# Kernel tuning notes

Measured on AMD Instinct MI355X. Metric: run time of the kernel, lower is better.

Reference implementation:

```python
import jax, jax.numpy as jnp
import numpy as np

N_NODES = 20000
N_EDGES = 320000
N_GRAPHS = 64
OBS = 64
EDGE_DIM = 16
HEADS = 4
HID = 64
NEG_SLOPE = 0.2
EPS = 1e-16


def _gat_layer(x, src, dst, edge_attr, W, We, att_src, att_dst, att_edge, b):
    """PyG GATConv (concat=True, eval mode: no dropout).
    x: [N, Fin], edge_attr: [E, De], W: [Fin, H*C], We: [De, H*C],
    att_*: [H, C], b: [H*C]. Returns [N, H*C]."""
    N = x.shape[0]
    h = (x @ W).reshape(N, HEADS, HID)                      # [N,H,C]
    he = (edge_attr @ We).reshape(-1, HEADS, HID)           # [E,H,C]
    a_src = jnp.einsum('nhc,hc->nh', h, att_src)            # [N,H]
    a_dst = jnp.einsum('nhc,hc->nh', h, att_dst)
    a_e = jnp.einsum('ehc,hc->eh', he, att_edge)            # [E,H]
    alpha = a_src[src] + a_dst[dst] + a_e                   # [E,H]
    alpha = jax.nn.leaky_relu(alpha, NEG_SLOPE)
    # segment softmax over destination neighborhoods
    m = jax.ops.segment_max(alpha, dst, num_segments=N)     # [N,H]
    m = jnp.where(jnp.isfinite(m), m, 0.0)
    ea = jnp.exp(alpha - m[dst])
    denom = jax.ops.segment_sum(ea, dst, num_segments=N)    # [N,H]
    alpha = ea / (denom[dst] + EPS)
    msg = h[src] * alpha[:, :, None]                        # [E,H,C]
    out = jax.ops.segment_sum(msg, dst, num_segments=N)     # [N,H,C]
    return out.reshape(N, HEADS * HID) + b


def _make_params(key):
    ks = jax.random.split(key, 18)
    p = {}
    dims_in = [OBS, HEADS * HID, HEADS * HID]
    for i in range(3):
        j = i * 6
        fin = dims_in[i]
        p[f'W{i+1}'] = jax.random.normal(ks[j], (fin, HEADS * HID), jnp.float32) * (1.0 / np.sqrt(fin))
        p[f'We{i+1}'] = jax.random.normal(ks[j+1], (EDGE_DIM, HEADS * HID), jnp.float32) * (1.0 / np.sqrt(EDGE_DIM))
        p[f'att_src{i+1}'] = jax.random.normal(ks[j+2], (HEADS, HID), jnp.float32) * 0.1
        p[f'att_dst{i+1}'] = jax.random.normal(ks[j+3], (HEADS, HID), jnp.float32) * 0.1
        p[f'att_edge{i+1}'] = jax.random.normal(ks[j+4], (HEADS, HID), jnp.float32) * 0.1
        p[f'b{i+1}'] = jnp.zeros((HEADS * HID,), jnp.float32)
    return p


def setup_inputs() -> dict:
    key = jax.random.key(0)
    k1, k2, k3, k4, kp = jax.random.split(key, 5)
    inp = {
        'x': jax.random.normal(k1, (N_NODES, OBS), jnp.float32),
        'edge_index': jax.random.randint(k2, (2, N_EDGES), 0, N_NODES, jnp.int64),
        'edge_attr': jax.random.normal(k3, (N_EDGES, EDGE_DIM), jnp.float32),
        'batch': jnp.sort(jax.random.randint(k4, (N_NODES,), 0, N_GRAPHS, jnp.int64)),
    }
    inp.update(_make_params(kp))
    return inp


def reference(x, edge_index, edge_attr, batch,
              W1, We1, att_src1, att_dst1, att_edge1, b1,
              W2, We2, att_src2, att_dst2, att_edge2, b2,
              W3, We3, att_src3, att_dst3, att_edge3, b3):
    src, dst = edge_index[0], edge_index[1]
    h = jax.nn.relu(_gat_layer(x, src, dst, edge_attr, W1, We1, att_src1, att_dst1, att_edge1, b1))
    h = jax.nn.relu(_gat_layer(h, src, dst, edge_attr, W2, We2, att_src2, att_dst2, att_edge2, b2))
    h = jax.nn.relu(_gat_layer(h, src, dst, edge_attr, W3, We3, att_src3, att_dst3, att_edge3, b3))
    # global mean pool over graphs
    sums = jax.ops.segment_sum(h, batch, num_segments=N_GRAPHS)      # [G, H*C]
    counts = jax.ops.segment_sum(jnp.ones((h.shape[0], 1), h.dtype), batch, num_segments=N_GRAPHS)
    pooled = sums / jnp.maximum(counts, 1.0)
    return jnp.tanh(pooled)
```

## Files before the change

kernel.cpp:

```cpp
#include <hip/hip_runtime.h>
#include <hip/hip_bf16.h>
#include <hip/hip_fp16.h>
#include <math.h>

#define N_NODES 20000
#define N_EDGES 320000
#define N_GRAPHS 64
#define OBS 64
#define EDGE_DIM 16
#define HEADS 4
#define HID 64
#define HC 256
#define NEG_SLOPE 0.2f
#define EPSF 1e-16f
#define N_SCAN_BLOCKS ((N_NODES + 255) / 256)
#define CVT_BLOCKS (N_NODES * OBS / 4 / 256)

typedef _Float16 f16x8 __attribute__((ext_vector_type(8)));
typedef float f32x4 __attribute__((ext_vector_type(4)));

__global__ __launch_bounds__(256) void zero3_kernel(int* __restrict__ counts,
                                                    float* __restrict__ pooled,
                                                    int* __restrict__ gcounts) {
    int i = blockIdx.x * 256 + threadIdx.x;
    if (i < N_NODES) counts[i] = 0;
    if (i < N_GRAPHS * HC) pooled[i] = 0.f;
    if (i < N_GRAPHS) gcounts[i] = 0;
}

__global__ __launch_bounds__(256) void cvtwt_kernel(const float* __restrict__ x, __half* __restrict__ x16,
                                                    const float* __restrict__ W0, const float* __restrict__ W1,
                                                    const float* __restrict__ W2,
                                                    __half* __restrict__ wt0, __half* __restrict__ wt1,
                                                    __half* __restrict__ wt2) {
    int b = blockIdx.x, t = threadIdx.x;
    if (b < CVT_BLOCKS) {
        int i = (b * 256 + t) * 4;
        float4 v = *(const float4*)(x + i);
        *(__half2*)(x16 + i)     = __floats2half2_rn(v.x, v.y);
        *(__half2*)(x16 + i + 2) = __floats2half2_rn(v.z, v.w);
    } else if (b < CVT_BLOCKS + OBS) {
        int k = b - CVT_BLOCKS;
        wt0[(size_t)t * OBS + k] = __float2half(W0[(size_t)k * HC + t]);
    } else if (b < CVT_BLOCKS + OBS + HC) {
        int k = b - CVT_BLOCKS - OBS;
        wt1[(size_t)t * HC + k] = __float2half(W1[(size_t)k * HC + t]);
    } else {
        int k = b - CVT_BLOCKS - OBS - HC;
        wt2[(size_t)t * HC + k] = __float2half(W2[(size_t)k * HC + t]);
    }
}

__global__ __launch_bounds__(256) void count_kernel(const int* __restrict__ ei, int* __restrict__ counts) {
    int e = blockIdx.x * 256 + threadIdx.x;
    if (e >= N_EDGES) return;
    atomicAdd(&counts[ei[N_EDGES + e]], 1);
}

__global__ __launch_bounds__(256) void scan_local_kernel(const int* __restrict__ counts,
                                                         int* __restrict__ row_start,
                                                         int* __restrict__ blk_tot) {
    int b = blockIdx.x, t = threadIdx.x;
    int i = b * 256 + t;
    int v = (i < N_NODES) ? counts[i] : 0;
    int lane = t & 63, w = t >> 6;
    int x = v;
    #pragma unroll
    for (int off = 1; off < 64; off <<= 1) {
        int y = __shfl_up(x, off, 64);
        if (lane >= off) x += y;
    }
    __shared__ int wsum[4];
    __shared__ int woff[4];
    if (lane == 63) wsum[w] = x;
    __syncthreads();
    if (t == 0) {
        int s = 0;
        #pragma unroll
        for (int k = 0; k < 4; ++k) { woff[k] = s; s += wsum[k]; }
        blk_tot[b] = s;
    }
    __syncthreads();
    if (i < N_NODES) row_start[i] = x - v + woff[w];
}

__global__ __launch_bounds__(256) void scan_add_kernel(int* __restrict__ row_start,
                                                       const int* __restrict__ blk_tot,
                                                       int* __restrict__ cursor) {
    __shared__ int sd[128];
    int b = blockIdx.x, t = threadIdx.x;
    if (t < 128) sd[t] = (t < b && t < N_SCAN_BLOCKS) ? blk_tot[t] : 0;
    __syncthreads();
    #pragma unroll
    for (int off = 64; off >= 1; off >>= 1) {
        if (t < off) sd[t] += sd[t + off];
        __syncthreads();
    }
    int base = sd[0];
    int i = b * 256 + t;
    if (i < N_NODES) {
        int r = row_start[i] + base;
        row_start[i] = r;
        cursor[i] = r;
    }
}

__global__ __launch_bounds__(256) void fill_kernel(const int* __restrict__ ei,
                                                   int* __restrict__ cursor,
                                                   int* __restrict__ src_csr,
                                                   int* __restrict__ edge_pos) {
    int e = blockIdx.x * 256 + threadIdx.x;
    if (e >= N_EDGES) return;
    int s = ei[e];
    int d = ei[N_EDGES + e];
    int pos = atomicAdd(&cursor[d], 1);
    src_csr[pos] = s;
    edge_pos[e] = pos;
}

__global__ void weff3_kernel(const float* __restrict__ We0, const float* __restrict__ ae0,
                             const float* __restrict__ We1, const float* __restrict__ ae1,
                             const float* __restrict__ We2, const float* __restrict__ ae2,
                             float* __restrict__ w_eff3) {
    int l = blockIdx.x, t = threadIdx.x;
    const float* We = (l == 0) ? We0 : (l == 1) ? We1 : We2;
    const float* ae = (l == 0) ? ae0 : (l == 1) ? ae1 : ae2;
    int hh = t >> 4, d = t & 15;
    float acc = 0.f;
    #pragma unroll 8
    for (int c = 0; c < HID; ++c)
        acc += We[d * HC + hh * HID + c] * ae[hh * HID + c];
    w_eff3[l * 64 + hh * 16 + d] = acc;
}

__global__ __launch_bounds__(256) void ae3_kernel(const float* __restrict__ edge_attr,
                                                  const int* __restrict__ edge_pos,
                                                  const float* __restrict__ w_eff3,
                                                  float4* __restrict__ ae_csr) {
    __shared__ float wsh[192];
    int t = threadIdx.x;
    if (t < 192) wsh[t] = w_eff3[t];
    __syncthreads();
    int e = blockIdx.x * 256 + t;
    if (e >= N_EDGES) return;
    const float* ea = edge_attr + (size_t)e * EDGE_DIM;
    float x[16];
    #pragma unroll
    for (int i = 0; i < 16; i += 4) {
        float4 v = *(const float4*)(ea + i);
        x[i] = v.x; x[i + 1] = v.y; x[i + 2] = v.z; x[i + 3] = v.w;
    }
    int pos = edge_pos[e];
    #pragma unroll
    for (int l = 0; l < 3; ++l) {
        float al[4];
        #pragma unroll
        for (int hh = 0; hh < 4; ++hh) {
            float acc = 0.f;
            #pragma unroll
            for (int i = 0; i < 16; ++i) acc += x[i] * wsh[l * 64 + hh * 16 + i];
            al[hh] = acc;
        }
        ae_csr[(size_t)l * N_EDGES + pos] = make_float4(al[0], al[1], al[2], al[3]);
    }
}

template <int NKT>
__global__ __launch_bounds__(256) void gemm16_kernel(const __half* __restrict__ A16,
                                                     const __half* __restrict__ Wt16,
                                                     __half* __restrict__ C16, int M,
                                                     const float* __restrict__ att_src,
                                                     const float* __restrict__ att_dst,
                                                     float* __restrict__ a_src,
                                                     float* __restrict__ a_dst) {
    constexpr int K = NKT * 32;
    __shared__ __align__(16) _Float16 lds[64 * 264];
    int t = threadIdx.x;
    int w = t >> 6, l = t & 63;
    int cg = l & 15, gg = l >> 4;
    int m0 = blockIdx.x * 64;

    {
        int row = (t >> 6) * 16 + (t & 15);
        int k8 = (t >> 4) & 3;
        int rg = m0 + row;
        if (rg >= M) rg = M - 1;
        const _Float16* ag = (const _Float16*)A16 + (size_t)rg * K + k8 * 8;
        f16x8 tmp[NKT];
        #pragma unroll
        for (int j = 0; j < NKT; ++j) tmp[j] = *(const f16x8*)(ag + j * 32);
        #pragma unroll
        for (int j = 0; j < NKT; ++j) *(f16x8*)&lds[(size_t)(j * 256 + t) * 8] = tmp[j];
    }
    __syncthreads();

    f32x4 acc[4][4] = {};
    const _Float16* bg = (const _Float16*)Wt16 + (size_t)(w * 64 + cg) * K + gg * 8;
    #pragma unroll 2
    for (int kt = 0; kt < NKT; ++kt) {
        f16x8 bf[4], af[4];
        #pragma unroll
        for (int ni = 0; ni < 4; ++ni)
            bf[ni] = *(const f16x8*)(bg + (size_t)(ni * 16) * K + kt * 32);
        #pragma unroll
        for (int mi = 0; mi < 4; ++mi)
            af[mi] = *(const f16x8*)&lds[(size_t)(kt * 256 + mi * 64 + l) * 8];
        #pragma unroll
        for (int mi = 0; mi < 4; ++mi)
            #pragma unroll
            for (int ni = 0; ni < 4; ++ni)
                acc[mi][ni] = __builtin_amdgcn_mfma_f32_16x16x32_f16(af[mi], bf[ni], acc[mi][ni], 0, 0, 0);
    }

    {
        float avs[4], avd[4];
        #pragma unroll
        for (int ni = 0; ni < 4; ++ni) {
            avs[ni] = att_src[w * 64 + ni * 16 + cg];
            avd[ni] = att_dst[w * 64 + ni * 16 + cg];
        }
        #pragma unroll
        for (int mi = 0; mi < 4; ++mi)
            #pragma unroll
            for (int reg = 0; reg < 4; ++reg) {
                float ps = acc[mi][0][reg] * avs[0] + acc[mi][1][reg] * avs[1]
                         + acc[mi][2][reg] * avs[2] + acc[mi][3][reg] * avs[3];
                float pd = acc[mi][0][reg] * avd[0] + acc[mi][1][reg] * avd[1]
                         + acc[mi][2][reg] * avd[2] + acc[mi][3][reg] * avd[3];
                #pragma unroll
                for (int o = 1; o < 16; o <<= 1) {
                    ps += __shfl_xor(ps, o, 64);
                    pd += __shfl_xor(pd, o, 64);
                }
                int m = m0 + mi * 16 + gg * 4 + reg;
                if (cg == 0 && m < M) {
                    a_src[(size_t)m * 4 + w] = ps;
                    a_dst[(size_t)m * 4 + w] = pd;
                }
            }
    }

    __syncthreads();
    #pragma unroll
    for (int mi = 0; mi < 4; ++mi)
        #pragma unroll
        for (int ni = 0; ni < 4; ++ni)
            #pragma unroll
            for (int reg = 0; reg < 4; ++reg) {
                int row = mi * 16 + gg * 4 + reg;
                int col = w * 64 + ni * 16 + cg;
                lds[row * 264 + col] = (_Float16)acc[mi][ni][reg];
            }
    __syncthreads();
    #pragma unroll
    for (int i = 0; i < 8; ++i) {
        int g = i * 256 + t;
        int row = g >> 5, cw = g & 31;
        int m = m0 + row;
        if (m < M) {
            f16x8 v = *(const f16x8*)&lds[row * 264 + cw * 8];
            *(f16x8*)((_Float16*)C16 + (size_t)m * HC + cw * 8) = v;
        }
    }
}

__global__ __launch_bounds__(256) void aggregate2_kernel(const int* __restrict__ src_csr,
                                                         const float4* __restrict__ ae_csr,
                                                         const int* __restrict__ row_start,
                                                         const int* __restrict__ counts,
                                                         const float* __restrict__ a_src,
                                                         const float* __restrict__ a_dst,
                                                         const __half* __restrict__ h16,
                                                         const float* __restrict__ bias,
                                                         __half* __restrict__ out16) {
    __shared__ float4 alds[4][64];
    int wid = threadIdx.x >> 6, lane = threadIdx.x & 63;
    int n = blockIdx.x * 4 + wid;
    int start = row_start[n];
    int deg = counts[n];
    const float4* ae = ae_csr + start;
    const int* sp = src_csr + start;
    float4 ad = *(const float4*)(a_dst + (size_t)n * 4);

    float m0 = -INFINITY, m1 = -INFINITY, m2 = -INFINITY, m3 = -INFINITY;
    for (int i = lane; i < deg; i += 64) {
        float4 a = ae[i];
        int s = sp[i];
        float4 as = *(const float4*)(a_src + (size_t)s * 4);
        float v0 = a.x + as.x + ad.x; v0 = v0 > 0.f ? v0 : NEG_SLOPE * v0;
        float v1 = a.y + as.y + ad.y; v1 = v1 > 0.f ? v1 : NEG_SLOPE * v1;
        float v2 = a.z + as.z + ad.z; v2 = v2 > 0.f ? v2 : NEG_SLOPE * v2;
        float v3 = a.w + as.w + ad.w; v3 = v3 > 0.f ? v3 : NEG_SLOPE * v3;
        if (i < 64) alds[wid][i] = make_float4(v0, v1, v2, v3);
        m0 = fmaxf(m0, v0); m1 = fmaxf(m1, v1);
        m2 = fmaxf(m2, v2); m3 = fmaxf(m3, v3);
    }
    #pragma unroll
    for (int o = 32; o > 0; o >>= 1) {
        m0 = fmaxf(m0, __shfl_xor(m0, o, 64));
        m1 = fmaxf(m1, __shfl_xor(m1, o, 64));
        m2 = fmaxf(m2, __shfl_xor(m2, o, 64));
        m3 = fmaxf(m3, __shfl_xor(m3, o, 64));
    }
    __syncthreads();

    bool lo = (lane < 32);
    float mA = lo ? m0 : m1;
    float mB = lo ? m2 : m3;

    float aAx = 0.f, aAy = 0.f, aBx = 0.f, aBy = 0.f;
    float dA = 0.f, dB = 0.f;
    int s_next = (deg > 0) ? sp[0] : 0;
    #pragma unroll 2
    for (int i = 0; i < deg; ++i) {
        int s = s_next;
        if (i + 1 < deg) s_next = sp[i + 1];
        float4 al;
        if (i < 64) {
            al = alds[wid][i];
        } else {
            float4 a = ae[i];
            float4 as = *(const float4*)(a_src + (size_t)s * 4);
            al.x = a.x + as.x + ad.x; al.x = al.x > 0.f ? al.x : NEG_SLOPE * al.x;
            al.y = a.y + as.y + ad.y; al.y = al.y > 0.f ? al.y : NEG_SLOPE * al.y;
            al.z = a.z + as.z + ad.z; al.z = al.z > 0.f ? al.z : NEG_SLOPE * al.z;
            al.w = a.w + as.w + ad.w; al.w = al.w > 0.f ? al.w : NEG_SLOPE * al.w;
        }
        float eA = __expf((lo ? al.x : al.y) - mA);
        float eB = __expf((lo ? al.z : al.w) - mB);
        dA += eA; dB += eB;
        const __half2* hr = (const __half2*)(h16 + (size_t)s * HC);
        __half2 vA = hr[lane];
        __half2 vB = hr[64 + lane];
        float2 fA = __half22float2(vA);
        float2 fB = __half22float2(vB);
        aAx += eA * fA.x; aAy += eA * fA.y;
        aBx += eB * fB.x; aBy += eB * fB.y;
    }
    float2 b01 = *(const float2*)(bias + 2 * lane);
    float2 b23 = *(const float2*)(bias + 128 + 2 * lane);
    float invA = 1.f / (dA + EPSF);
    float invB = 1.f / (dB + EPSF);
    float r0 = fmaxf(aAx * invA + b01.x, 0.f);
    float r1 = fmaxf(aAy * invA + b01.y, 0.f);
    float r2 = fmaxf(aBx * invB + b23.x, 0.f);
    float r3 = fmaxf(aBy * invB + b23.y, 0.f);
    __half* o = out16 + (size_t)n * HC;
    *(__half2*)(o + 2 * lane)       = __floats2half2_rn(r0, r1);
    *(__half2*)(o + 128 + 2 * lane) = __floats2half2_rn(r2, r3);
}

#define NPB 100
__global__ __launch_bounds__(256) void pool_kernel(const __half* __restrict__ h,
                                                   const int* __restrict__ batch,
                                                   float* __restrict__ pooled,
                                                   int* __restrict__ gcounts) {
    int t = threadIdx.x;
    int n0 = blockIdx.x * NPB;
    int n1 = n0 + NPB;
    if (n1 > N_NODES) n1 = N_NODES;
    if (n0 >= N_NODES) return;
    int cur = batch[n0];
    float acc = 0.f;
    int cnt = 0;
    for (int n = n0; n < n1; ++n) {
        int g = batch[n];
        if (g != cur) {
            atomicAdd(&pooled[cur * HC + t], acc);
            if (t == 0) atomicAdd(&gcounts[cur], cnt);
            acc = 0.f; cnt = 0; cur = g;
        }
        acc += __half2float(h[(size_t)n * HC + t]);
        cnt++;
    }
    atomicAdd(&pooled[cur * HC + t], acc);
    if (t == 0) atomicAdd(&gcounts[cur], cnt);
}

__global__ __launch_bounds__(256) void finalize_kernel(const float* __restrict__ pooled,
                                                       const int* __restrict__ gcounts,
                                                       float* __restrict__ out) {
    int g = blockIdx.x, t = threadIdx.x;
    float c = (float)(gcounts[g] > 1 ? gcounts[g] : 1);
    out[g * HC + t] = tanhf(pooled[g * HC + t] / c);
}

extern "C" void kernel_launch(void* const* d_in, const int* in_sizes, int n_in,
                              void* d_out, int out_size, void* d_ws, size_t ws_size,
                              hipStream_t stream) {
    const float* x         = (const float*)d_in[0];
    const int*   ei        = (const int*)d_in[1];
    const float* edge_attr = (const float*)d_in[2];
    const int*   batch     = (const int*)d_in[3];
    const float* Wl[3]  = {(const float*)d_in[4],  (const float*)d_in[10], (const float*)d_in[16]};
    const float* Wel[3] = {(const float*)d_in[5],  (const float*)d_in[11], (const float*)d_in[17]};
    const float* asl[3] = {(const float*)d_in[6],  (const float*)d_in[12], (const float*)d_in[18]};
    const float* adl[3] = {(const float*)d_in[7],  (const float*)d_in[13], (const float*)d_in[19]};
    const float* ael[3] = {(const float*)d_in[8],  (const float*)d_in[14], (const float*)d_in[20]};
    const float* bl[3]  = {(const float*)d_in[9],  (const float*)d_in[15], (const float*)d_in[21]};
    float* out = (float*)d_out;

    char* p = (char*)d_ws;
    auto alloc = [&](size_t bytes) -> void* {
        void* r = (void*)p;
        p += (bytes + 255) & ~(size_t)255;
        return r;
    };
    __half* x16       = (__half*)alloc((size_t)N_NODES * OBS * 2);
    __half* hA16      = (__half*)alloc((size_t)N_NODES * HC * 2);
    __half* hB16      = (__half*)alloc((size_t)N_NODES * HC * 2);
    __half* wt0       = (__half*)alloc((size_t)HC * OBS * 2);
    __half* wt1       = (__half*)alloc((size_t)HC * HC * 2);
    __half* wt2       = (__half*)alloc((size_t)HC * HC * 2);
    float* a_src      = (float*)alloc((size_t)N_NODES * 4 * 4);
    float* a_dst      = (float*)alloc((size_t)N_NODES * 4 * 4);
    float4* ae_csr    = (float4*)alloc((size_t)3 * N_EDGES * 16);
    int* counts       = (int*)alloc((size_t)N_NODES * 4);
    int* row_start    = (int*)alloc((size_t)N_NODES * 4);
    int* cursor       = (int*)alloc((size_t)N_NODES * 4);
    int* src_csr      = (int*)alloc((size_t)N_EDGES * 4);
    int* edge_pos     = (int*)alloc((size_t)N_EDGES * 4);
    float* w_eff3     = (float*)alloc(192 * 4);
    float* pooled     = (float*)alloc((size_t)N_GRAPHS * HC * 4);
    int* gcounts      = (int*)alloc((size_t)N_GRAPHS * 4);
    int* blk_tot      = (int*)alloc((size_t)N_SCAN_BLOCKS * 4);

    zero3_kernel<<<N_SCAN_BLOCKS, 256, 0, stream>>>(counts, pooled, gcounts);
    cvtwt_kernel<<<CVT_BLOCKS + OBS + HC + HC, 256, 0, stream>>>(x, x16, Wl[0], Wl[1], Wl[2],
                                                                 wt0, wt1, wt2);
    weff3_kernel<<<3, 64, 0, stream>>>(Wel[0], ael[0], Wel[1], ael[1], Wel[2], ael[2], w_eff3);

    count_kernel<<<N_EDGES / 256, 256, 0, stream>>>(ei, counts);
    scan_local_kernel<<<N_SCAN_BLOCKS, 256, 0, stream>>>(counts, row_start, blk_tot);
    scan_add_kernel<<<N_SCAN_BLOCKS, 256, 0, stream>>>(row_start, blk_tot, cursor);
    fill_kernel<<<N_EDGES / 256, 256, 0, stream>>>(ei, cursor, src_csr, edge_pos);

    ae3_kernel<<<N_EDGES / 256, 256, 0, stream>>>(edge_attr, edge_pos, w_eff3, ae_csr);

    const int ngrid = (N_NODES + 63) / 64;
    const __half* wtl[3] = {wt0, wt1, wt2};
    const __half* cur_in = x16;
    for (int l = 0; l < 3; ++l) {
        if (l == 0)
            gemm16_kernel<2><<<ngrid, 256, 0, stream>>>(cur_in, wtl[l], hA16, N_NODES,
                                                        asl[l], adl[l], a_src, a_dst);
        else
            gemm16_kernel<8><<<ngrid, 256, 0, stream>>>(cur_in, wtl[l], hA16, N_NODES,
                                                        asl[l], adl[l], a_src, a_dst);
        aggregate2_kernel<<<N_NODES / 4, 256, 0, stream>>>(src_csr, ae_csr + (size_t)l * N_EDGES,
                                                           row_start, counts, a_src, a_dst,
                                                           hA16, bl[l], hB16);
        cur_in = hB16;
    }

    pool_kernel<<<(N_NODES + NPB - 1) / NPB, 256, 0, stream>>>(hB16, batch, pooled, gcounts);
    finalize_kernel<<<N_GRAPHS, 256, 0, stream>>>(pooled, gcounts, out);
}
```

Measured before the change: 250.4 us.

## Split aggregation into parallel softmax pass and two-edge-per-wave gather

The aggregation kernel now computes the softmax denominators in a separate lane-parallel pass and stores the exponentiated weights in shared memory. The gather loop splits each wave into two half-waves that handle alternate edges. Each lane loads 8 fp16 features per edge with one 16-byte load, and the two halves are combined with a shuffle. This is meant to halve the serial edge-loop length and widen memory accesses per lane, at the cost of an extra reduction pass and a duplicated tail iteration for odd degrees.

After: 244.5 us. 1.02x faster.

```diff
diff --git a/kernel.cpp b/kernel.cpp
--- a/kernel.cpp
+++ b/kernel.cpp
@@ -15,6 +15,7 @@
 #define EPSF 1e-16f
 #define N_SCAN_BLOCKS ((N_NODES + 255) / 256)
 #define CVT_BLOCKS (N_NODES * OBS / 4 / 256)
+#define CAP 64
 
 typedef _Float16 f16x8 __attribute__((ext_vector_type(8)));
 typedef float f32x4 __attribute__((ext_vector_type(4)));
@@ -264,7 +265,7 @@
     }
 }
 
-__global__ __launch_bounds__(256) void aggregate2_kernel(const int* __restrict__ src_csr,
+__global__ __launch_bounds__(256) void aggregate3_kernel(const int* __restrict__ src_csr,
                                                          const float4* __restrict__ ae_csr,
                                                          const int* __restrict__ row_start,
                                                          const int* __restrict__ counts,
@@ -273,7 +274,7 @@
                                                          const __half* __restrict__ h16,
                                                          const float* __restrict__ bias,
                                                          __half* __restrict__ out16) {
-    __shared__ float4 alds[4][64];
+    __shared__ float wlds[4][4][CAP + 1];
     int wid = threadIdx.x >> 6, lane = threadIdx.x & 63;
     int n = blockIdx.x * 4 + wid;
     int start = row_start[n];
@@ -291,7 +292,10 @@
         float v1 = a.y + as.y + ad.y; v1 = v1 > 0.f ? v1 : NEG_SLOPE * v1;
         float v2 = a.z + as.z + ad.z; v2 = v2 > 0.f ? v2 : NEG_SLOPE * v2;
         float v3 = a.w + as.w + ad.w; v3 = v3 > 0.f ? v3 : NEG_SLOPE * v3;
-        if (i < 64) alds[wid][i] = make_float4(v0, v1, v2, v3);
+        if (i < CAP) {
+            wlds[wid][0][i] = v0; wlds[wid][1][i] = v1;
+            wlds[wid][2][i] = v2; wlds[wid][3][i] = v3;
+        }
         m0 = fmaxf(m0, v0); m1 = fmaxf(m1, v1);
         m2 = fmaxf(m2, v2); m3 = fmaxf(m3, v3);
     }
@@ -302,52 +306,91 @@
         m2 = fmaxf(m2, __shfl_xor(m2, o, 64));
         m3 = fmaxf(m3, __shfl_xor(m3, o, 64));
     }
-    __syncthreads();
-
-    bool lo = (lane < 32);
-    float mA = lo ? m0 : m1;
-    float mB = lo ? m2 : m3;
-
-    float aAx = 0.f, aAy = 0.f, aBx = 0.f, aBy = 0.f;
-    float dA = 0.f, dB = 0.f;
-    int s_next = (deg > 0) ? sp[0] : 0;
-    #pragma unroll 2
-    for (int i = 0; i < deg; ++i) {
-        int s = s_next;
-        if (i + 1 < deg) s_next = sp[i + 1];
-        float4 al;
-        if (i < 64) {
-            al = alds[wid][i];
+
+    float d0 = 0.f, d1 = 0.f, d2 = 0.f, d3 = 0.f;
+    for (int i = lane; i < deg; i += 64) {
+        float v0, v1, v2, v3;
+        if (i < CAP) {
+            v0 = wlds[wid][0][i]; v1 = wlds[wid][1][i];
+            v2 = wlds[wid][2][i]; v3 = wlds[wid][3][i];
         } else {
             float4 a = ae[i];
+            int s = sp[i];
             float4 as = *(const float4*)(a_src + (size_t)s * 4);
-            al.x = a.x + as.x + ad.x; al.x = al.x > 0.f ? al.x : NEG_SLOPE * al.x;
-            al.y = a.y + as.y + ad.y; al.y = al.y > 0.f ? al.y : NEG_SLOPE * al.y;
-            al.z = a.z + as.z + ad.z; al.z = al.z > 0.f ? al.z : NEG_SLOPE * al.z;
-            al.w = a.w + as.w + ad.w; al.w = al.w > 0.f ? al.w : NEG_SLOPE * al.w;
-        }
-        float eA = __expf((lo ? al.x : al.y) - mA);
-        float eB = __expf((lo ? al.z : al.w) - mB);
-        dA += eA; dB += eB;
-        const __half2* hr = (const __half2*)(h16 + (size_t)s * HC);
-        __half2 vA = hr[lane];
-        __half2 vB = hr[64 + lane];
-        float2 fA = __half22float2(vA);
-        float2 fB = __half22float2(vB);
-        aAx += eA * fA.x; aAy += eA * fA.y;
-        aBx += eB * fB.x; aBy += eB * fB.y;
-    }
-    float2 b01 = *(const float2*)(bias + 2 * lane);
-    float2 b23 = *(const float2*)(bias + 128 + 2 * lane);
-    float invA = 1.f / (dA + EPSF);
-    float invB = 1.f / (dB + EPSF);
-    float r0 = fmaxf(aAx * invA + b01.x, 0.f);
-    float r1 = fmaxf(aAy * invA + b01.y, 0.f);
-    float r2 = fmaxf(aBx * invB + b23.x, 0.f);
-    float r3 = fmaxf(aBy * invB + b23.y, 0.f);
-    __half* o = out16 + (size_t)n * HC;
-    *(__half2*)(o + 2 * lane)       = __floats2half2_rn(r0, r1);
-    *(__half2*)(o + 128 + 2 * lane) = __floats2half2_rn(r2, r3);
+            v0 = a.x + as.x + ad.x; v0 = v0 > 0.f ? v0 : NEG_SLOPE * v0;
+            v1 = a.y + as.y + ad.y; v1 = v1 > 0.f ? v1 : NEG_SLOPE * v1;
+            v2 = a.z + as.z + ad.z; v2 = v2 > 0.f ? v2 : NEG_SLOPE * v2;
+            v3 = a.w + as.w + ad.w; v3 = v3 > 0.f ? v3 : NEG_SLOPE * v3;
+        }
+        float e0 = __expf(v0 - m0);
+        float e1 = __expf(v1 - m1);
+        float e2 = __expf(v2 - m2);
+        float e3 = __expf(v3 - m3);
+        d0 += e0; d1 += e1; d2 += e2; d3 += e3;
+        if (i < CAP) {
+            wlds[wid][0][i] = e0; wlds[wid][1][i] = e1;
+            wlds[wid][2][i] = e2; wlds[wid][3][i] = e3;
+        }
+    }
+    #pragma unroll
+    for (int o = 32; o > 0; o >>= 1) {
+        d0 += __shfl_xor(d0, o, 64);
+        d1 += __shfl_xor(d1, o, 64);
+        d2 += __shfl_xor(d2, o, 64);
+        d3 += __shfl_xor(d3, o, 64);
+    }
+
+    int g = lane >> 5, j = lane & 31;
+    int head = j >> 3;
+    float mh = (head < 2) ? (head == 0 ? m0 : m1) : (head == 2 ? m2 : m3);
+    float dh = (head < 2) ? (head == 0 ? d0 : d1) : (head == 2 ? d2 : d3);
+    float adh = (head < 2) ? (head == 0 ? ad.x : ad.y) : (head == 2 ? ad.z : ad.w);
+
+    float acc[8] = {};
+    int niter = (deg + 1) >> 1;
+    #pragma unroll 2
+    for (int it = 0; it < niter; ++it) {
+        int e = it * 2 + g;
+        bool valid = e < deg;
+        int ec = valid ? e : deg - 1;
+        int s = sp[ec];
+        float wgt;
+        if (ec < CAP) {
+            wgt = wlds[wid][head][ec];
+        } else {
+            float4 a = ae[ec];
+            float aa = (head < 2) ? (head == 0 ? a.x : a.y) : (head == 2 ? a.z : a.w);
+            const float* asp = a_src + (size_t)s * 4;
+            float v = aa + asp[head] + adh;
+            v = v > 0.f ? v : NEG_SLOPE * v;
+            wgt = __expf(v - mh);
+        }
+        if (!valid) wgt = 0.f;
+        f16x8 hv = *(const f16x8*)((const _Float16*)h16 + (size_t)s * HC + j * 8);
+        #pragma unroll
+        for (int q = 0; q < 8; ++q) acc[q] += wgt * (float)hv[q];
+    }
+    #pragma unroll
+    for (int q = 0; q < 8; ++q) acc[q] += __shfl_xor(acc[q], 32, 64);
+
+    if (g == 0) {
+        float invd = 1.f / (dh + EPSF);
+        float4 b0 = *(const float4*)(bias + j * 8);
+        float4 b1 = *(const float4*)(bias + j * 8 + 4);
+        float r[8];
+        r[0] = fmaxf(acc[0] * invd + b0.x, 0.f);
+        r[1] = fmaxf(acc[1] * invd + b0.y, 0.f);
+        r[2] = fmaxf(acc[2] * invd + b0.z, 0.f);
+        r[3] = fmaxf(acc[3] * invd + b0.w, 0.f);
+        r[4] = fmaxf(acc[4] * invd + b1.x, 0.f);
+        r[5] = fmaxf(acc[5] * invd + b1.y, 0.f);
+        r[6] = fmaxf(acc[6] * invd + b1.z, 0.f);
+        r[7] = fmaxf(acc[7] * invd + b1.w, 0.f);
+        f16x8 o;
+        #pragma unroll
+        for (int q = 0; q < 8; ++q) o[q] = (_Float16)r[q];
+        *(f16x8*)((_Float16*)out16 + (size_t)n * HC + j * 8) = o;
+    }
 }
 
 #define NPB 100
@@ -447,7 +490,7 @@
         else
             gemm16_kernel<8><<<ngrid, 256, 0, stream>>>(cur_in, wtl[l], hA16, N_NODES,
                                                         asl[l], adl[l], a_src, a_dst);
-        aggregate2_kernel<<<N_NODES / 4, 256, 0, stream>>>(src_csr, ae_csr + (size_t)l * N_EDGES,
+        aggregate3_kernel<<<N_NODES / 4, 256, 0, stream>>>(src_csr, ae_csr + (size_t)l * N_EDGES,
                                                            row_start, counts, a_src, a_dst,
                                                            hA16, bl[l], hB16);
         cur_in = hB16;
```
